# Kernel optimization log

Hardware: AMD Instinct MI355X
Metric: run time of the kernel (lower is better)

Reference implementation:

```python
import jax, jax.numpy as jnp
import numpy as np

HEADS = 8
DIM = 32  # dim_heads


def setup_inputs() -> dict:
    key = jax.random.key(0)
    k1, k2, k3, k4 = jax.random.split(key, 4)
    b, c, h, w = 8, 256, 128, 128
    hidden = HEADS * DIM  # 256
    x = jax.random.normal(k1, (b, c, h, w), dtype=jnp.float32)
    w_qkv = jax.random.normal(k2, (3 * hidden, c), dtype=jnp.float32) * 0.05
    w_out = jax.random.normal(k3, (c, hidden), dtype=jnp.float32) * 0.05
    b_out = jax.random.normal(k4, (c,), dtype=jnp.float32) * 0.05
    return {"x": x, "w_qkv": w_qkv, "w_out": w_out, "b_out": b_out}


def reference(x, w_qkv, w_out, b_out):
    b, c, h, w = x.shape
    n = h * w
    # 1x1 conv == channel matmul: [b, 3*heads*dim, h, w]
    qkv = jnp.einsum('bchw,oc->bohw', x, w_qkv)
    # rearrange 'b (qkv heads c) h w -> qkv b heads c (h w)'
    qkv = qkv.reshape(b, 3, HEADS, DIM, n)
    q, k, v = qkv[:, 0], qkv[:, 1], qkv[:, 2]  # each [b, heads, dim, n]
    k = jax.nn.softmax(k, axis=-1)
    # context: [b, heads, dim, dim]
    context = jnp.einsum('bhdn,bhen->bhde', k, v)
    o = jnp.einsum('bhde,bhdn->bhen', context, q)  # [b, heads, dim, n]
    o = o.reshape(b, HEADS * DIM, h, w)
    # out 1x1 conv with bias
    o = jnp.einsum('bchw,oc->bohw', o, w_out) + b_out[None, :, None, None]
    return o
```

## Files before the change

kernel.cpp:

```cpp
#include <hip/hip_runtime.h>
#include <hip/hip_bf16.h>
#include <cstdint>

#define NPIX 16384
#define BATCH 8
#define CDIM 256

typedef __bf16 bh8 __attribute__((ext_vector_type(8)));
typedef __bf16 bh4 __attribute__((ext_vector_type(4)));
typedef float  fx4 __attribute__((ext_vector_type(4)));

__device__ __forceinline__ void gload16(const void* g, void* l) {
  __builtin_amdgcn_global_load_lds(
      (const __attribute__((address_space(1))) uint32_t*)g,
      (__attribute__((address_space(3))) uint32_t*)l, 16, 0, 0);
}

__device__ __forceinline__ fx4 mfma16(bh8 a, bh8 b, fx4 c) {
  return __builtin_amdgcn_mfma_f32_16x16x32_bf16(a, b, c, 0, 0, 0);
}

__device__ __forceinline__ void pbar() {
  asm volatile("" ::: "memory");
  __builtin_amdgcn_s_barrier();
  asm volatile("" ::: "memory");
}
#define VMWI(n) asm volatile("s_waitcnt vmcnt(" #n ")" ::: "memory")

__global__ __launch_bounds__(256) void prep_w(const float* __restrict__ w_qkv,
                                              __bf16* __restrict__ wqb,
                                              __bf16* __restrict__ wqT) {
  __shared__ float tile[32][33];
  int bid = blockIdx.x;
  if (bid < 512) {
    int i = bid * 256 + threadIdx.x;
    wqb[i] = (__bf16)w_qkv[256 * 256 + i];
  } else {
    bid -= 512;
    const int t0 = (bid & 7) * 32, o0 = (bid >> 3) * 32;
    const int tx = threadIdx.x & 31, ty = threadIdx.x >> 5;
#pragma unroll
    for (int j = 0; j < 4; ++j) {
      int r = ty * 4 + j;
      tile[r][tx] = w_qkv[(size_t)(o0 + r) * 256 + t0 + tx];
    }
    __syncthreads();
#pragma unroll
    for (int j = 0; j < 4; ++j) {
      int tl = ty * 4 + j;
      wqT[(size_t)(t0 + tl) * 256 + o0 + tx] = (__bf16)tile[tx][tl];
    }
  }
}

__global__ __launch_bounds__(256) void transpose_x(const float* __restrict__ x,
                                                   __bf16* __restrict__ xT) {
  __shared__ float tf[64][68];
  const int n0 = blockIdx.x * 64, c0 = blockIdx.y * 64, b = blockIdx.z;
  const int u = threadIdx.x;
#pragma unroll
  for (int i = 0; i < 4; ++i) {
    int j = i * 256 + u;
    int r = j >> 4, q = j & 15;
    *(fx4*)&tf[r][q * 4] =
        *(const fx4*)&x[((size_t)b * CDIM + c0 + r) * NPIX + n0 + q * 4];
  }
  __syncthreads();
  const int nl = u >> 2, cq = (u & 3) * 16;
#pragma unroll
  for (int w = 0; w < 2; ++w) {
    bh8 v;
#pragma unroll
    for (int j = 0; j < 8; ++j) v[j] = (__bf16)tf[cq + w * 8 + j][nl];
    *(bh8*)&xT[((size_t)b * NPIX + n0 + nl) * CDIM + c0 + cq + w * 8] = v;
  }
}


#define BSP(pb) ((__bf16*)(smem + 32768 + (pb)*16384))

#define STA(kt)                                                                \
  do {                                                                         \
    _Pragma("unroll") for (int i_ = 0; i_ < 4; ++i_) {                         \
      int j_ = i_ * 512 + tid;                                                 \
      int row_ = j_ >> 3, c_ = j_ & 7;                                         \
      int sc_ = c_ ^ (row_ & 7);                                               \
      const __bf16* sb_;                                                       \
      if (EPI == 0) sb_ = (i_ < 2) ? Abk + (size_t)row_ * 256                  \
                                   : Abv + (size_t)(row_ - 128) * 256;         \
      else          sb_ = Ab + (size_t)row_ * 256;                             \
      gload16(sb_ + (kt)*64 + sc_ * 8, As + j_ * 8);                           \
    }                                                                          \
  } while (0)

#define STB(kt, pb)                                                            \
  do {                                                                         \
    _Pragma("unroll") for (int i_ = 0; i_ < 2; ++i_) {                         \
      int j_ = i_ * 512 + tid;                                                 \
      int row_ = j_ >> 3, c_ = j_ & 7;                                         \
      int sc_ = c_ ^ (row_ & 7);                                               \
      gload16(Bb + (size_t)row_ * 256 + (kt)*64 + sc_ * 8, BSP(pb) + j_ * 8);  \
    }                                                                          \
  } while (0)

#define COMP(pb)                                                               \
  do {                                                                         \
    _Pragma("unroll") for (int ks_ = 0; ks_ < 2; ++ks_) {                      \
      bh8 a_[4], b_[4];                                                        \
      const int swk_ = (ks_ * 4 + fq) ^ (fr & 7);                              \
      _Pragma("unroll") for (int m_ = 0; m_ < 4; ++m_)                         \
        a_[m_] = *(const bh8*)&As[(wm * 64 + m_ * 16 + fr) * 64 + swk_ * 8];   \
      _Pragma("unroll") for (int n_ = 0; n_ < 4; ++n_)                         \
        b_[n_] = *(const bh8*)&BSP(pb)[(wn * 64 + n_ * 16 + fr) * 64 + swk_ * 8];\
      _Pragma("unroll") for (int m_ = 0; m_ < 4; ++m_)                         \
      _Pragma("unroll") for (int n_ = 0; n_ < 4; ++n_)                         \
        acc[m_][n_] = mfma16(a_[m_], b_[n_], acc[m_][n_]);                     \
    }                                                                          \
  } while (0)

template <int EPI>
__global__ __launch_bounds__(512, 4) void gemm256(
    const __bf16* __restrict__ A, const __bf16* __restrict__ Bx,
    float* __restrict__ S_part, float* __restrict__ Zpart,
    const float* __restrict__ bias, float* __restrict__ fout) {
  __shared__ __align__(16) char smem[66560];
  __bf16* As = (__bf16*)smem;
  const int tid = threadIdx.x;
  const int bx = (EPI == 0) ? blockIdx.y : blockIdx.x;
  const int by = (EPI == 0) ? blockIdx.x : blockIdx.y;
  const int b = blockIdx.z;
  const int lane = tid & 63, wid = tid >> 6;
  const int wm = wid >> 1, wn = wid & 1;
  const int fr = lane & 15, fq = lane >> 4;
  const int hg = by * 4;
  const __bf16* Abk = A + (size_t)(hg * 32) * 256;
  const __bf16* Abv = A + (size_t)(256 + hg * 32) * 256;
  const __bf16* Ab  = A + (size_t)b * 65536;
  const __bf16* Bb = Bx + ((size_t)b * NPIX + (size_t)bx * 128) * 256;

  fx4 acc[4][4] = {};

  STB(0, 0); STA(0);
  STB(1, 1); VMWI(2); pbar(); COMP(0); pbar(); STA(1);
  STB(2, 0); VMWI(2); pbar(); COMP(1); pbar(); STA(2);
  STB(3, 1); VMWI(2); pbar(); COMP(0); pbar(); STA(3);
             VMWI(0); pbar(); COMP(1); pbar();

  if (EPI == 0) {
    float* zrow = (float*)(smem + 65536);
    if (tid < 128) zrow[tid] = 0.f;
#pragma unroll
    for (int m = 0; m < 4; ++m)
#pragma unroll
      for (int n = 0; n < 4; ++n)
#pragma unroll
        for (int j = 0; j < 4; ++j) {
          int r = wm * 64 + m * 16 + fq * 4 + j;
          int px = wn * 64 + n * 16 + fr;
          int pc = px >> 3;
          if (wm < 2) {
            int byo = r * 256 + ((pc ^ (r & 7)) << 4) + (px & 7) * 2;
            *(__bf16*)(smem + byo) = (__bf16)__expf(acc[m][n][j]);
          } else {
            int r2 = r - 128;
            int byo = r2 * 256 + ((pc ^ (r2 & 7)) << 4) + (px & 7) * 2;
            *(__bf16*)(smem + 32768 + byo) = (__bf16)acc[m][n][j];
          }
        }
    __syncthreads();
    {
      int r = tid >> 2, c0 = (tid & 3) * 32;
      float za = 0.f;
#pragma unroll
      for (int i2 = 0; i2 < 4; ++i2) {
        int px0 = c0 + i2 * 8;
        int pc = px0 >> 3;
        bh8 ev = *(const bh8*)(smem + r * 256 + ((pc ^ (r & 7)) << 4));
#pragma unroll
        for (int jj = 0; jj < 8; ++jj) za += (float)ev[jj];
      }
      atomicAdd(&zrow[r], za);
    }
    fx4 sac0 = {}, sac1 = {};
#pragma unroll
    for (int t2 = 0; t2 < 2; ++t2) {
      int tk = wid * 2 + t2;
      int hl = tk >> 2, quad = tk & 3;
      int drow = (quad >> 1) * 16, erow = (quad & 1) * 16;
      fx4 sac = {};
#pragma unroll
      for (int kt2 = 0; kt2 < 4; ++kt2) {
        int ra = hl * 32 + drow + fr;
        int rb = hl * 32 + erow + fr;
        int pc = kt2 * 4 + fq;
        bh8 af = *(const bh8*)(smem + ra * 256 + ((pc ^ (ra & 7)) << 4));
        bh8 bf = *(const bh8*)(smem + 32768 + rb * 256 + ((pc ^ (rb & 7)) << 4));
        sac = mfma16(af, bf, sac);
      }
      if (t2 == 0) sac0 = sac; else sac1 = sac;
    }
    __syncthreads();
    float* Sb = (float*)smem;
#pragma unroll
    for (int t2 = 0; t2 < 2; ++t2) {
      int tk = wid * 2 + t2;
      int hl = tk >> 2, quad = tk & 3;
      int drow = (quad >> 1) * 16, erow = (quad & 1) * 16;
      fx4 sv = (t2 == 0) ? sac0 : sac1;
#pragma unroll
      for (int j = 0; j < 4; ++j)
        Sb[hl * 1024 + (drow + fq * 4 + j) * 32 + erow + fr] = sv[j];
    }
    __syncthreads();
    {
      int hl = tid >> 7, idx = tid & 127;
      float* sp = S_part + ((size_t)((b * 8 + hg + hl) * 128 + bx)) * 1024;
      fx4 v0 = *(const fx4*)&Sb[hl * 1024 + idx * 8];
      fx4 v1 = *(const fx4*)&Sb[hl * 1024 + idx * 8 + 4];
      *(fx4*)&sp[idx * 8] = v0;
      *(fx4*)&sp[idx * 8 + 4] = v1;
    }
    if (tid < 128) {
      int head = hg + (tid >> 5);
      Zpart[((size_t)(b * 8 + head) * 128 + bx) * 32 + (tid & 31)] = zrow[tid];
    }
  } else {
    const size_t obase = (size_t)b * CDIM * NPIX + (size_t)bx * 128;
    float* Ls = (float*)smem;
#pragma unroll
    for (int m = 0; m < 4; ++m) {
      __syncthreads();
#pragma unroll
      for (int n = 0; n < 4; ++n)
#pragma unroll
        for (int j = 0; j < 4; ++j)
          Ls[(wm * 16 + fq * 4 + j) * 132 + wn * 64 + n * 16 + fr] =
              acc[m][n][j] + bias[wm * 64 + m * 16 + fq * 4 + j];
      __syncthreads();
#pragma unroll
      for (int it = 0; it < 4; ++it) {
        int u = it * 512 + tid;
        int rr = u >> 5, cc = u & 31;
        int gch = (rr >> 4) * 64 + m * 16 + (rr & 15);
        fx4 val = *(const fx4*)&Ls[rr * 132 + cc * 4];
        *(fx4*)&fout[obase + (size_t)gch * NPIX + cc * 4] = val;
      }
    }
  }
}

__global__ __launch_bounds__(256) void reduce_ctx(const float* __restrict__ S_part,
                                                  const float* __restrict__ Zpart,
                                                  float* __restrict__ ctx) {
  const int seg = blockIdx.x;
  const int bh = blockIdx.y;
  const int t = threadIdx.x;
  __shared__ float zs[8];
  if (t < 8) zs[t] = 0.f;
  __syncthreads();
  {
    int row = seg * 8 + (t >> 5);
    float z = 0.f;
    for (int ch = (t & 31); ch < 128; ch += 32)
      z += Zpart[((size_t)bh * 128 + ch) * 32 + row];
    atomicAdd(&zs[t >> 5], z);
  }
  __syncthreads();
  const int i = seg * 256 + t;
  float s = 0.f;
  for (int ch = 0; ch < 128; ++ch) s += S_part[((size_t)bh * 128 + ch) * 1024 + i];
  ctx[(size_t)bh * 1024 + i] = s / zs[t >> 5];
}

__global__ __launch_bounds__(256) void make_w2(const float* __restrict__ ctx,
                                               const float* __restrict__ w_out,
                                               __bf16* __restrict__ W2b) {
  const int oc = blockIdx.x, b = blockIdx.y, t = threadIdx.x;
  const int h = t >> 5, d = t & 31;
  const float* wrow = w_out + oc * 256 + h * 32;
  const float* crow = ctx + (((size_t)b * 8 + h) * 32 + d) * 32;
  float s = 0.f;
#pragma unroll
  for (int e = 0; e < 32; ++e) s += wrow[e] * crow[e];
  W2b[((size_t)b * 256 + oc) * 256 + t] = (__bf16)s;
}

__global__ __launch_bounds__(256) void make_w3(const __bf16* __restrict__ W2b,
                                               const __bf16* __restrict__ wqT,
                                               __bf16* __restrict__ W3) {
  const int bx = blockIdx.x, by = blockIdx.y, b = blockIdx.z;
  const int lane = threadIdx.x & 63, wid = threadIdx.x >> 6;
  const int wm = wid >> 1, wn = wid & 1;
  const int fr = lane & 15, fq = lane >> 4;
  const __bf16* Ab = W2b + (size_t)b * 65536 + (size_t)(by * 128 + wm * 64) * 256;
  const __bf16* Bb = wqT + (size_t)(bx * 128 + wn * 64) * 256;
  fx4 acc[4][4] = {};
#pragma unroll
  for (int h = 0; h < 8; ++h) {
    bh8 a_[4], b_[4];
#pragma unroll
    for (int m = 0; m < 4; ++m)
      a_[m] = *(const bh8*)(Ab + (size_t)(m * 16 + fr) * 256 + h * 32 + fq * 8);
#pragma unroll
    for (int n = 0; n < 4; ++n)
      b_[n] = *(const bh8*)(Bb + (size_t)(n * 16 + fr) * 256 + h * 32 + fq * 8);
#pragma unroll
    for (int m = 0; m < 4; ++m)
#pragma unroll
      for (int n = 0; n < 4; ++n) acc[m][n] = mfma16(a_[m], b_[n], acc[m][n]);
  }
#pragma unroll
  for (int m = 0; m < 4; ++m)
#pragma unroll
    for (int n = 0; n < 4; ++n) {
      int r0 = by * 128 + wm * 64 + m * 16 + fq * 4;
      int t0 = bx * 128 + wn * 64 + n * 16 + fr;
#pragma unroll
      for (int j = 0; j < 4; ++j)
        W3[(size_t)b * 65536 + (size_t)(r0 + j) * 256 + t0] = (__bf16)acc[m][n][j];
    }
}

extern "C" void kernel_launch(void* const* d_in, const int* in_sizes, int n_in,
                              void* d_out, int out_size, void* d_ws, size_t ws_size,
                              hipStream_t stream) {
  const float* x     = (const float*)d_in[0];
  const float* w_qkv = (const float*)d_in[1];
  const float* w_out = (const float*)d_in[2];
  const float* b_out = (const float*)d_in[3];
  float* out = (float*)d_out;

  char* ws = (char*)d_ws;
  __bf16* xT    = (__bf16*)(ws);
  __bf16* wqb   = (__bf16*)(ws + 67108864ull);
  __bf16* wqT   = (__bf16*)(ws + 67371008ull);
  __bf16* W2b   = (__bf16*)(ws + 67502080ull);
  __bf16* W3    = (__bf16*)(ws + 68550656ull);
  float*  S_part= (float*) (ws + 69599232ull);
  float*  Zpart = (float*) (ws + 103153664ull);
  float*  ctx   = (float*) (ws + 104202240ull);

  prep_w<<<576, 256, 0, stream>>>(w_qkv, wqb, wqT);
  transpose_x<<<dim3(NPIX / 64, CDIM / 64, BATCH), 256, 0, stream>>>(x, xT);
  gemm256<0><<<dim3(2, NPIX / 128, BATCH), 512, 0, stream>>>(
      wqb, xT, S_part, Zpart, nullptr, nullptr);
  reduce_ctx<<<dim3(4, 64), 256, 0, stream>>>(S_part, Zpart, ctx);
  make_w2<<<dim3(256, BATCH), 256, 0, stream>>>(ctx, w_out, W2b);
  make_w3<<<dim3(2, 2, BATCH), 256, 0, stream>>>(W2b, wqT, W3);
  gemm256<1><<<dim3(NPIX / 128, 1, BATCH), 512, 0, stream>>>(
      W3, xT, nullptr, nullptr, b_out, out);
}
```

Measured before the change: 178.5 us.

## Shrink GEMM tiles to 128x128 with 256-thread blocks and single-buffered staging

Both GEMM kernels now use 128x128 output tiles with 4 waves instead of 256x128 with 8 waves. The LDS footprint roughly halves and the double-buffered B pipeline is dropped: each k-step loads A and B, waits, then computes. The grids double in the head or channel dimension. This aims for more resident blocks per CU and a smaller footprint, but it loses load/compute overlap and re-reads the xT tiles twice as often.

```diff
diff --git a/kernel.cpp b/kernel.cpp
--- a/kernel.cpp
+++ b/kernel.cpp
@@ -77,41 +77,42 @@
 }
 
 
-#define BSP(pb) ((__bf16*)(smem + 32768 + (pb)*16384))
+#define BSP ((__bf16*)(smem + 16384))
 
 #define STA(kt)                                                                \
   do {                                                                         \
     _Pragma("unroll") for (int i_ = 0; i_ < 4; ++i_) {                         \
-      int j_ = i_ * 512 + tid;                                                 \
+      int j_ = i_ * 256 + tid;                                                 \
       int row_ = j_ >> 3, c_ = j_ & 7;                                         \
       int sc_ = c_ ^ (row_ & 7);                                               \
       const __bf16* sb_;                                                       \
       if (EPI == 0) sb_ = (i_ < 2) ? Abk + (size_t)row_ * 256                  \
-                                   : Abv + (size_t)(row_ - 128) * 256;         \
+                                   : Abv + (size_t)(row_ - 64) * 256;          \
       else          sb_ = Ab + (size_t)row_ * 256;                             \
-      gload16(sb_ + (kt)*64 + sc_ * 8, As + j_ * 8);                           \
+      gload16(sb_ + (kt)*64 + sc_ * 8, (__bf16*)smem + j_ * 8);                \
     }                                                                          \
   } while (0)
 
-#define STB(kt, pb)                                                            \
+#define STB(kt)                                                                \
   do {                                                                         \
-    _Pragma("unroll") for (int i_ = 0; i_ < 2; ++i_) {                         \
-      int j_ = i_ * 512 + tid;                                                 \
+    _Pragma("unroll") for (int i_ = 0; i_ < 4; ++i_) {                         \
+      int j_ = i_ * 256 + tid;                                                 \
       int row_ = j_ >> 3, c_ = j_ & 7;                                         \
       int sc_ = c_ ^ (row_ & 7);                                               \
-      gload16(Bb + (size_t)row_ * 256 + (kt)*64 + sc_ * 8, BSP(pb) + j_ * 8);  \
+      gload16(Bb + (size_t)row_ * 256 + (kt)*64 + sc_ * 8, BSP + j_ * 8);      \
     }                                                                          \
   } while (0)
 
-#define COMP(pb)                                                               \
+#define COMP()                                                                 \
   do {                                                                         \
     _Pragma("unroll") for (int ks_ = 0; ks_ < 2; ++ks_) {                      \
       bh8 a_[4], b_[4];                                                        \
       const int swk_ = (ks_ * 4 + fq) ^ (fr & 7);                              \
       _Pragma("unroll") for (int m_ = 0; m_ < 4; ++m_)                         \
-        a_[m_] = *(const bh8*)&As[(wm * 64 + m_ * 16 + fr) * 64 + swk_ * 8];   \
+        a_[m_] = *(const bh8*)&((__bf16*)smem)[(wm * 64 + m_ * 16 + fr) * 64 + \
+                                               swk_ * 8];                      \
       _Pragma("unroll") for (int n_ = 0; n_ < 4; ++n_)                         \
-        b_[n_] = *(const bh8*)&BSP(pb)[(wn * 64 + n_ * 16 + fr) * 64 + swk_ * 8];\
+        b_[n_] = *(const bh8*)&BSP[(wn * 64 + n_ * 16 + fr) * 64 + swk_ * 8];  \
       _Pragma("unroll") for (int m_ = 0; m_ < 4; ++m_)                         \
       _Pragma("unroll") for (int n_ = 0; n_ < 4; ++n_)                         \
         acc[m_][n_] = mfma16(a_[m_], b_[n_], acc[m_][n_]);                     \
@@ -119,62 +120,56 @@
   } while (0)
 
 template <int EPI>
-__global__ __launch_bounds__(512, 4) void gemm256(
+__global__ __launch_bounds__(256, 3) void gemm256(
     const __bf16* __restrict__ A, const __bf16* __restrict__ Bx,
     float* __restrict__ S_part, float* __restrict__ Zpart,
     const float* __restrict__ bias, float* __restrict__ fout) {
-  __shared__ __align__(16) char smem[66560];
-  __bf16* As = (__bf16*)smem;
+  __shared__ __align__(16) char smem[33024];
   const int tid = threadIdx.x;
-  const int bx = (EPI == 0) ? blockIdx.y : blockIdx.x;
-  const int by = (EPI == 0) ? blockIdx.x : blockIdx.y;
+  const int by = blockIdx.x;
+  const int bx = blockIdx.y;
   const int b = blockIdx.z;
   const int lane = tid & 63, wid = tid >> 6;
   const int wm = wid >> 1, wn = wid & 1;
   const int fr = lane & 15, fq = lane >> 4;
-  const int hg = by * 4;
-  const __bf16* Abk = A + (size_t)(hg * 32) * 256;
-  const __bf16* Abv = A + (size_t)(256 + hg * 32) * 256;
-  const __bf16* Ab  = A + (size_t)b * 65536;
+  const int hp = by;
+  const __bf16* Abk = A + (size_t)(hp * 64) * 256;
+  const __bf16* Abv = A + (size_t)(256 + hp * 64) * 256;
+  const __bf16* Ab  = A + (size_t)b * 65536 + (size_t)by * 128 * 256;
   const __bf16* Bb = Bx + ((size_t)b * NPIX + (size_t)bx * 128) * 256;
 
   fx4 acc[4][4] = {};
 
-  STB(0, 0); STA(0);
-  STB(1, 1); VMWI(2); pbar(); COMP(0); pbar(); STA(1);
-  STB(2, 0); VMWI(2); pbar(); COMP(1); pbar(); STA(2);
-  STB(3, 1); VMWI(2); pbar(); COMP(0); pbar(); STA(3);
-             VMWI(0); pbar(); COMP(1); pbar();
+  STA(0); STB(0); VMWI(0); pbar(); COMP(); pbar();
+  STA(1); STB(1); VMWI(0); pbar(); COMP(); pbar();
+  STA(2); STB(2); VMWI(0); pbar(); COMP(); pbar();
+  STA(3); STB(3); VMWI(0); pbar(); COMP(); pbar();
 
   if (EPI == 0) {
-    float* zrow = (float*)(smem + 65536);
-    if (tid < 128) zrow[tid] = 0.f;
+    float* zrow = (float*)(smem + 32768);
+    if (tid < 64) zrow[tid] = 0.f;
 #pragma unroll
     for (int m = 0; m < 4; ++m)
 #pragma unroll
       for (int n = 0; n < 4; ++n)
 #pragma unroll
         for (int j = 0; j < 4; ++j) {
-          int r = wm * 64 + m * 16 + fq * 4 + j;
+          int r = m * 16 + fq * 4 + j;
           int px = wn * 64 + n * 16 + fr;
           int pc = px >> 3;
-          if (wm < 2) {
-            int byo = r * 256 + ((pc ^ (r & 7)) << 4) + (px & 7) * 2;
+          int byo = r * 256 + ((pc ^ (r & 7)) << 4) + (px & 7) * 2;
+          if (wm == 0)
             *(__bf16*)(smem + byo) = (__bf16)__expf(acc[m][n][j]);
-          } else {
-            int r2 = r - 128;
-            int byo = r2 * 256 + ((pc ^ (r2 & 7)) << 4) + (px & 7) * 2;
-            *(__bf16*)(smem + 32768 + byo) = (__bf16)acc[m][n][j];
-          }
+          else
+            *(__bf16*)(smem + 16384 + byo) = (__bf16)acc[m][n][j];
         }
-    __syncthreads();
+    pbar();
     {
       int r = tid >> 2, c0 = (tid & 3) * 32;
       float za = 0.f;
 #pragma unroll
       for (int i2 = 0; i2 < 4; ++i2) {
-        int px0 = c0 + i2 * 8;
-        int pc = px0 >> 3;
+        int pc = (c0 + i2 * 8) >> 3;
         bh8 ev = *(const bh8*)(smem + r * 256 + ((pc ^ (r & 7)) << 4));
 #pragma unroll
         for (int jj = 0; jj < 8; ++jj) za += (float)ev[jj];
@@ -194,12 +189,12 @@
         int rb = hl * 32 + erow + fr;
         int pc = kt2 * 4 + fq;
         bh8 af = *(const bh8*)(smem + ra * 256 + ((pc ^ (ra & 7)) << 4));
-        bh8 bf = *(const bh8*)(smem + 32768 + rb * 256 + ((pc ^ (rb & 7)) << 4));
+        bh8 bf = *(const bh8*)(smem + 16384 + rb * 256 + ((pc ^ (rb & 7)) << 4));
         sac = mfma16(af, bf, sac);
       }
       if (t2 == 0) sac0 = sac; else sac1 = sac;
     }
-    __syncthreads();
+    pbar();
     float* Sb = (float*)smem;
 #pragma unroll
     for (int t2 = 0; t2 < 2; ++t2) {
@@ -214,18 +209,19 @@
     __syncthreads();
     {
       int hl = tid >> 7, idx = tid & 127;
-      float* sp = S_part + ((size_t)((b * 8 + hg + hl) * 128 + bx)) * 1024;
+      float* sp = S_part + ((size_t)((b * 8 + hp * 2 + hl) * 128 + bx)) * 1024;
       fx4 v0 = *(const fx4*)&Sb[hl * 1024 + idx * 8];
       fx4 v1 = *(const fx4*)&Sb[hl * 1024 + idx * 8 + 4];
       *(fx4*)&sp[idx * 8] = v0;
       *(fx4*)&sp[idx * 8 + 4] = v1;
     }
-    if (tid < 128) {
-      int head = hg + (tid >> 5);
+    if (tid < 64) {
+      int head = hp * 2 + (tid >> 5);
       Zpart[((size_t)(b * 8 + head) * 128 + bx) * 32 + (tid & 31)] = zrow[tid];
     }
   } else {
-    const size_t obase = (size_t)b * CDIM * NPIX + (size_t)bx * 128;
+    const size_t obase =
+        (size_t)b * CDIM * NPIX + (size_t)(by * 128) * NPIX + (size_t)bx * 128;
     float* Ls = (float*)smem;
 #pragma unroll
     for (int m = 0; m < 4; ++m) {
@@ -235,11 +231,11 @@
 #pragma unroll
         for (int j = 0; j < 4; ++j)
           Ls[(wm * 16 + fq * 4 + j) * 132 + wn * 64 + n * 16 + fr] =
-              acc[m][n][j] + bias[wm * 64 + m * 16 + fq * 4 + j];
+              acc[m][n][j] + bias[by * 128 + wm * 64 + m * 16 + fq * 4 + j];
       __syncthreads();
 #pragma unroll
       for (int it = 0; it < 4; ++it) {
-        int u = it * 512 + tid;
+        int u = it * 256 + tid;
         int rr = u >> 5, cc = u & 31;
         int gch = (rr >> 4) * 64 + m * 16 + (rr & 15);
         fx4 val = *(const fx4*)&Ls[rr * 132 + cc * 4];
@@ -342,11 +338,11 @@
 
   prep_w<<<576, 256, 0, stream>>>(w_qkv, wqb, wqT);
   transpose_x<<<dim3(NPIX / 64, CDIM / 64, BATCH), 256, 0, stream>>>(x, xT);
-  gemm256<0><<<dim3(2, NPIX / 128, BATCH), 512, 0, stream>>>(
+  gemm256<0><<<dim3(4, NPIX / 128, BATCH), 256, 0, stream>>>(
       wqb, xT, S_part, Zpart, nullptr, nullptr);
   reduce_ctx<<<dim3(4, 64), 256, 0, stream>>>(S_part, Zpart, ctx);
   make_w2<<<dim3(256, BATCH), 256, 0, stream>>>(ctx, w_out, W2b);
   make_w3<<<dim3(2, 2, BATCH), 256, 0, stream>>>(W2b, wqT, W3);
-  gemm256<1><<<dim3(NPIX / 128, 1, BATCH), 512, 0, stream>>>(
+  gemm256<1><<<dim3(2, NPIX / 128, BATCH), 256, 0, stream>>>(
       W3, xT, nullptr, nullptr, b_out, out);
 }
```

New measurement: 176.0 us. Within noise of the previous version (-1.4%).
